# Kernel optimization log

Hardware: AMD Instinct MI355X
Metric: run time of the kernel (lower is better)

## Reference

```python
import jax, jax.numpy as jnp
import numpy as np

NU = 100_000   # users
NI = 100_000   # items
D  = 64        # embedding_size
NR = 1_000_000 # rate edges (user->item)
NL = 500_000   # link edges (user->user)
NEG_SLOPE = 0.2


def setup_inputs() -> dict:
    key = jax.random.key(0)
    ks = iter(jax.random.split(key, 40))
    s1 = 1.0 / np.sqrt(D)      # fan-in D
    s2 = 1.0 / np.sqrt(2 * D)  # fan-in 2D
    def nrm(shape, scale):
        return (jax.random.normal(next(ks), shape, jnp.float32) * scale).astype(jnp.float32)
    def idx(n, hi):
        return jax.random.randint(next(ks), (n,), 0, hi, jnp.int32)
    inp = {
        "user_emb": nrm((NU, D), 0.1),
        "item_emb": nrm((NI, D), 0.1),
        "rate_src": idx(NR, NU), "rate_dst": idx(NR, NI),
        "link_src": idx(NL, NU), "link_dst": idx(NL, NU),
        "neg_rate_src": idx(NR, NU), "neg_rate_dst": idx(NR, NI),
        "neg_link_src": idx(NL, NU), "neg_link_dst": idx(NL, NU),
        "lambda_max": jnp.full((), 2.0, jnp.float32),
        "gat_Wsrc": nrm((5, D, D), s1), "gat_bsrc": nrm((5, D), s1),
        "gat_Wdst": nrm((5, D, D), s1), "gat_bdst": nrm((5, D), s1),
        "gat_attn": nrm((5, D), s1),
        "W_out": nrm((2 * D, D), s2), "b_out": nrm((D,), s2),
        "cheb_W": nrm((3, D, D), s1), "cheb_b": nrm((D,), s1),
        "Wc": nrm((2 * D, D), s2), "bc": nrm((D,), s2),
        "Ws": nrm((2 * D, D), s2), "bs": nrm((D,), s2),
        "WpP": nrm((2 * D, D), s2), "bpP": nrm((D,), s2),
        "WpS": nrm((2 * D, D), s2), "bpS": nrm((D,), s2),
    }
    return inp


def _gatv2(Wsrc, bsrc, Wdst, bdst, attn, h_src, h_dst, src, dst, n_dst):
    """DGL GATv2Conv, num_heads=1, head dim squeezed. Returns [n_dst, D]."""
    fs = h_src @ Wsrc + bsrc            # [Ns, D]
    fd = h_dst @ Wdst + bdst            # [Nd, D]
    e = jax.nn.leaky_relu(fs[src] + fd[dst], NEG_SLOPE)  # [E, D]
    s = e @ attn                        # [E]
    m = jax.ops.segment_max(s, dst, num_segments=n_dst)
    ex = jnp.exp(s - m[dst])
    den = jax.ops.segment_sum(ex, dst, num_segments=n_dst)
    alpha = ex / den[dst]               # edge softmax per dst node
    return jax.ops.segment_sum(alpha[:, None] * fs[src], dst, num_segments=n_dst)


def _forward(user_emb, item_emb, rate_src, rate_dst, link_src, link_dst,
             neg_rate_src, neg_rate_dst, neg_link_src, neg_link_dst,
             lambda_max, gat_Wsrc, gat_bsrc, gat_Wdst, gat_bdst, gat_attn,
             W_out, b_out, cheb_W, cheb_b, Wc, bc, Ws, bs, WpP, bpP, WpS, bpS):
    def gat(i, h_src, h_dst, src, dst, n_dst):
        return _gatv2(gat_Wsrc[i], gat_bsrc[i], gat_Wdst[i], gat_bdst[i],
                      gat_attn[i], h_src, h_dst, src, dst, n_dst)

    # ---- SpatialAttentionLayer_GAT ----
    h1_item = gat(0, user_emb, item_emb, rate_src, rate_dst, NI)      # layer1[rate]
    h2_user = gat(1, item_emb, user_emb, rate_dst, rate_src, NU)      # layer1[rated-by]
    item_infl = gat(2, h1_item, user_emb, rate_dst, rate_src, NU)     # layer2[rated-by]
    social_item = gat(3, h2_user, user_emb, link_src, link_dst, NU)   # layer2[link]
    user_pref = jnp.concatenate([item_infl, social_item], axis=1) @ W_out + b_out

    # ---- SpectralAttentionLayer: ChebConv(k=3) on social graph + GATv2 ----
    indeg = jax.ops.segment_sum(jnp.ones((NL,), jnp.float32), link_dst, num_segments=NU)
    dinv = jnp.maximum(indeg, 1.0) ** -0.5
    def ahat(x):  # D^{-1/2} A D^{-1/2} x over link edges
        msg = (x * dinv[:, None])[link_src]
        return dinv[:, None] * jax.ops.segment_sum(msg, link_dst, num_segments=NU)
    re = 2.0 / lambda_max
    T0 = user_emb
    rst = T0 @ cheb_W[0]
    h = ahat(T0)
    T1 = -re * h + T0 * (re - 1.0)
    rst = rst + T1 @ cheb_W[1]
    h = ahat(T1)
    T2 = -2.0 * re * h + 2.0 * (re - 1.0) * T1 - T0
    rst = rst + T2 @ cheb_W[2] + cheb_b
    user_social = gat(4, rst, rst, link_src, link_dst, NU)

    # ---- MutualisicLayer ----
    h_uP = jnp.concatenate([user_pref, user_emb], axis=1) @ Wc + bc
    h_uS = jnp.concatenate([user_social, user_emb], axis=1) @ Ws + bs
    h_m = h_uP * h_uS
    h_mP = h_m * jax.nn.softmax(h_uP, axis=1)
    h_mS = h_m * jax.nn.softmax(h_uS, axis=1)
    h_miu_mP = jnp.concatenate([h_mP, h_uP], axis=1)
    h_miu_mS = jnp.concatenate([h_mS, h_uS], axis=1)

    # ---- PredictionLayer ----
    h_new_P = h_miu_mP @ WpP + bpP
    h_new_S = h_miu_mS @ WpS + bpS

    # ---- HeteroDotProductPredictor (u_dot_v per edge) ----
    pos_rate = jnp.sum(h_new_P[rate_src] * item_emb[rate_dst], axis=-1)
    neg_rate = jnp.sum(h_new_P[neg_rate_src] * item_emb[neg_rate_dst], axis=-1)
    pos_link = jnp.sum(h_new_S[link_src] * user_emb[link_dst], axis=-1)
    neg_link = jnp.sum(h_new_S[neg_link_src] * user_emb[neg_link_dst], axis=-1)
    return pos_rate, neg_rate, pos_link, neg_link


def reference(user_emb, item_emb, rate_src, rate_dst, link_src, link_dst,
              neg_rate_src, neg_rate_dst, neg_link_src, neg_link_dst,
              lambda_max, gat_Wsrc, gat_bsrc, gat_Wdst, gat_bdst, gat_attn,
              W_out, b_out, cheb_W, cheb_b, Wc, bc, Ws, bs, WpP, bpP, WpS, bpS):
    return _forward(user_emb, item_emb, rate_src, rate_dst, link_src, link_dst,
                    neg_rate_src, neg_rate_dst, neg_link_src, neg_link_dst,
                    lambda_max, gat_Wsrc, gat_bsrc, gat_Wdst, gat_bdst, gat_attn,
                    W_out, b_out, cheb_W, cheb_b, Wc, bc, Ws, bs, WpP, bpP, WpS, bpS)
```

## Files before the change

### kernel.cpp

```cpp
#include <hip/hip_runtime.h>


#define LRELU_SLOPE 0.2f
#define MFMA_BLOCKS 1024
#define EDGE_BLOCKS 2048

typedef unsigned short u16;
typedef unsigned int uint32;
typedef __attribute__((ext_vector_type(8))) short short8;
typedef __attribute__((ext_vector_type(4))) float f32x4;

__device__ __forceinline__ float b2f(u16 u) {
  return __uint_as_float(((uint32)u) << 16);
}
__device__ __forceinline__ u16 f2b(float f) {
  uint32 u = __float_as_uint(f);
  uint32 r = (u + 0x7fffu + ((u >> 16) & 1u)) >> 16;
  return (u16)r;
}
__device__ __forceinline__ float blo(uint32 p) { return __uint_as_float(p << 16); }
__device__ __forceinline__ float bhi(uint32 p) { return __uint_as_float(p & 0xffff0000u); }
__device__ __forceinline__ uint32 packb(float lo, float hi) {
  return (uint32)f2b(lo) | ((uint32)f2b(hi) << 16);
}

__global__ void cvt_k(const float4* __restrict__ X, ushort4* __restrict__ Y, int n4) {
  const int stride = gridDim.x * blockDim.x;
  for (int i = blockIdx.x * blockDim.x + threadIdx.x; i < n4; i += stride) {
    const float4 v = X[i];
    ushort4 o;
    o.x = f2b(v.x); o.y = f2b(v.y); o.z = f2b(v.z); o.w = f2b(v.w);
    Y[i] = o;
  }
}

__global__ void wfrag_k(const float* __restrict__ W, u16* __restrict__ fb, int nmat) {
  const int total = nmat * 4096;
  const int stride = gridDim.x * blockDim.x;
  for (int i = blockIdx.x * blockDim.x + threadIdx.x; i < total; i += stride) {
    const int mat = i >> 12, rem = i & 4095;
    const int l = rem >> 6, r = rem & 63;
    const int kc = r >> 5, cb = (r >> 3) & 3, j = r & 7;
    const int k = kc * 32 + ((l >> 4) & 3) * 8 + j;
    const int col = cb * 16 + (l & 15);
    fb[i] = f2b(W[(size_t)mat * 4096 + k * 64 + col]);
  }
}

template <int NIN>
__global__ void mfma_g_k(const u16* __restrict__ X0, const u16* __restrict__ X1,
                         const u16* __restrict__ X2,
                         const u16* __restrict__ F0, const u16* __restrict__ F1,
                         const u16* __restrict__ F2,
                         const float* __restrict__ b, u16* __restrict__ Y, int N) {
  const int lane = threadIdx.x & 63;
  const int gw = (blockIdx.x * blockDim.x + threadIdx.x) >> 6;
  const int nw = (gridDim.x * blockDim.x) >> 6;
  const int lo = lane & 15, hi = lane >> 4;
  short8 bf[NIN][2][4];
#pragma unroll
  for (int i = 0; i < NIN; ++i) {
    const u16* Fi = (i == 0) ? F0 : ((i == 1) ? F1 : F2);
#pragma unroll
    for (int kc = 0; kc < 2; ++kc)
#pragma unroll
      for (int cb = 0; cb < 4; ++cb)
        bf[i][kc][cb] = *(const short8*)(Fi + (size_t)lane * 64 + kc * 32 + cb * 8);
  }
  float bcol[4];
#pragma unroll
  for (int cb = 0; cb < 4; ++cb) bcol[cb] = b[cb * 16 + lo];
  const int ntile = (N + 15) >> 4;
  for (int t = gw; t < ntile; t += nw) {
    int arow = t * 16 + lo;
    if (arow >= N) arow = N - 1;
    f32x4 acc[4];
#pragma unroll
    for (int cb = 0; cb < 4; ++cb) {
      acc[cb][0] = bcol[cb]; acc[cb][1] = bcol[cb];
      acc[cb][2] = bcol[cb]; acc[cb][3] = bcol[cb];
    }
#pragma unroll
    for (int i = 0; i < NIN; ++i) {
      const u16* Xi = (i == 0) ? X0 : ((i == 1) ? X1 : X2);
      const short8 a0 = *(const short8*)(Xi + (size_t)arow * 64 + hi * 8);
      const short8 a1 = *(const short8*)(Xi + (size_t)arow * 64 + 32 + hi * 8);
#pragma unroll
      for (int cb = 0; cb < 4; ++cb)
        acc[cb] = __builtin_amdgcn_mfma_f32_16x16x32_bf16(a0, bf[i][0][cb], acc[cb], 0, 0, 0);
#pragma unroll
      for (int cb = 0; cb < 4; ++cb)
        acc[cb] = __builtin_amdgcn_mfma_f32_16x16x32_bf16(a1, bf[i][1][cb], acc[cb], 0, 0, 0);
    }
#pragma unroll
    for (int cb = 0; cb < 4; ++cb) {
#pragma unroll
      for (int j = 0; j < 4; ++j) {
        const int row = t * 16 + hi * 4 + j;
        if (row < N) Y[(size_t)row * 64 + cb * 16 + lo] = f2b(acc[cb][j]);
      }
    }
  }
}

__global__ void mfma_g2_k(const u16* __restrict__ X,
                          const u16* __restrict__ F0, const u16* __restrict__ F1,
                          const float* __restrict__ b0, const float* __restrict__ b1,
                          u16* __restrict__ Y0, u16* __restrict__ Y1, int N) {
  const int lane = threadIdx.x & 63;
  const int gw = (blockIdx.x * blockDim.x + threadIdx.x) >> 6;
  const int nw = (gridDim.x * blockDim.x) >> 6;
  const int lo = lane & 15, hi = lane >> 4;
  short8 bfA[2][4], bfB[2][4];
#pragma unroll
  for (int kc = 0; kc < 2; ++kc)
#pragma unroll
    for (int cb = 0; cb < 4; ++cb) {
      bfA[kc][cb] = *(const short8*)(F0 + (size_t)lane * 64 + kc * 32 + cb * 8);
      bfB[kc][cb] = *(const short8*)(F1 + (size_t)lane * 64 + kc * 32 + cb * 8);
    }
  float bc0[4], bc1[4];
#pragma unroll
  for (int cb = 0; cb < 4; ++cb) { bc0[cb] = b0[cb * 16 + lo]; bc1[cb] = b1[cb * 16 + lo]; }
  const int ntile = (N + 15) >> 4;
  for (int t = gw; t < ntile; t += nw) {
    int arow = t * 16 + lo;
    if (arow >= N) arow = N - 1;
    const short8 a0 = *(const short8*)(X + (size_t)arow * 64 + hi * 8);
    const short8 a1 = *(const short8*)(X + (size_t)arow * 64 + 32 + hi * 8);
    f32x4 accA[4], accB[4];
#pragma unroll
    for (int cb = 0; cb < 4; ++cb) {
      accA[cb][0] = bc0[cb]; accA[cb][1] = bc0[cb]; accA[cb][2] = bc0[cb]; accA[cb][3] = bc0[cb];
      accB[cb][0] = bc1[cb]; accB[cb][1] = bc1[cb]; accB[cb][2] = bc1[cb]; accB[cb][3] = bc1[cb];
    }
#pragma unroll
    for (int cb = 0; cb < 4; ++cb) {
      accA[cb] = __builtin_amdgcn_mfma_f32_16x16x32_bf16(a0, bfA[0][cb], accA[cb], 0, 0, 0);
      accA[cb] = __builtin_amdgcn_mfma_f32_16x16x32_bf16(a1, bfA[1][cb], accA[cb], 0, 0, 0);
      accB[cb] = __builtin_amdgcn_mfma_f32_16x16x32_bf16(a0, bfB[0][cb], accB[cb], 0, 0, 0);
      accB[cb] = __builtin_amdgcn_mfma_f32_16x16x32_bf16(a1, bfB[1][cb], accB[cb], 0, 0, 0);
    }
#pragma unroll
    for (int cb = 0; cb < 4; ++cb) {
#pragma unroll
      for (int j = 0; j < 4; ++j) {
        const int row = t * 16 + hi * 4 + j;
        if (row < N) {
          Y0[(size_t)row * 64 + cb * 16 + lo] = f2b(accA[cb][j]);
          Y1[(size_t)row * 64 + cb * 16 + lo] = f2b(accB[cb][j]);
        }
      }
    }
  }
}

__global__ void hist_k(const int* __restrict__ key, int* __restrict__ cnt, int E) {
  const int e = blockIdx.x * blockDim.x + threadIdx.x;
  if (e < E) atomicAdd(cnt + key[e], 1);
}

__global__ void scan1_k(const int* __restrict__ in, int* __restrict__ out,
                        int* __restrict__ bsum, int n) {
  __shared__ int tmp[256];
  const int t = threadIdx.x;
  const int base = blockIdx.x * 1024 + t * 4;
  int v0 = (base + 0 < n) ? in[base + 0] : 0;
  int v1 = (base + 1 < n) ? in[base + 1] : 0;
  int v2 = (base + 2 < n) ? in[base + 2] : 0;
  int v3 = (base + 3 < n) ? in[base + 3] : 0;
  const int s = v0 + v1 + v2 + v3;
  tmp[t] = s;
  __syncthreads();
  for (int off = 1; off < 256; off <<= 1) {
    const int x = (t >= off) ? tmp[t - off] : 0;
    __syncthreads();
    tmp[t] += x;
    __syncthreads();
  }
  const int excl = tmp[t] - s;
  if (t == 255) bsum[blockIdx.x] = tmp[255];
  if (base + 0 < n) out[base + 0] = excl;
  if (base + 1 < n) out[base + 1] = excl + v0;
  if (base + 2 < n) out[base + 2] = excl + v0 + v1;
  if (base + 3 < n) out[base + 3] = excl + v0 + v1 + v2;
}
__global__ void scan2_k(int* __restrict__ bsum, int nb) {
  if (threadIdx.x == 0) {
    int acc = 0;
    for (int i = 0; i < nb; ++i) { const int v = bsum[i]; bsum[i] = acc; acc += v; }
  }
}
__global__ void scan3_k(int* __restrict__ out, const int* __restrict__ bsum, int n) {
  const int i = blockIdx.x * blockDim.x + threadIdx.x;
  if (i < n) out[i] += bsum[i >> 10];
}

__global__ void scatter_k(const int* __restrict__ key, const int* __restrict__ other,
                          int* __restrict__ cursor, int* __restrict__ srt, int E) {
  const int e = blockIdx.x * blockDim.x + threadIdx.x;
  if (e < E) {
    const int p = atomicAdd(cursor + key[e], 1);
    srt[p] = other[e];
  }
}

__global__ void gat32_k(const u16* __restrict__ fs, const u16* __restrict__ fd,
                        const float* __restrict__ attn,
                        const int* __restrict__ rowptr, const int* __restrict__ nbr,
                        u16* __restrict__ out, int N) {
  const int lane = threadIdx.x & 63;
  const int l = lane & 31, half = lane >> 5;
  const int wid = (blockIdx.x * blockDim.x + threadIdx.x) >> 6;
  const int nw = (gridDim.x * blockDim.x) >> 6;
  const float awlo = attn[2 * l], awhi = attn[2 * l + 1];
  const uint32* fs32 = (const uint32*)fs;
  const uint32* fd32 = (const uint32*)fd;
  uint32* out32 = (uint32*)out;
  for (int n0 = wid * 2; n0 < N; n0 += nw * 2) {
    const int n = n0 + half;
    const bool act = n < N;
    const int beg = act ? rowptr[n] : 0;
    const int end = act ? rowptr[n + 1] : 0;
    float fdlo = 0.0f, fdhi = 0.0f;
    if (act) {
      const uint32 fp = fd32[(size_t)n * 32 + l];
      fdlo = blo(fp); fdhi = bhi(fp);
    }
    float aclo = 0.0f, achi = 0.0f, den = 0.0f;
    int e = beg;
    for (; e + 1 < end; e += 2) {
      const int s0 = nbr[e], s1 = nbr[e + 1];
      const uint32 f0 = fs32[(size_t)s0 * 32 + l];
      const uint32 f1 = fs32[(size_t)s1 * 32 + l];
      const float f0l = blo(f0), f0h = bhi(f0);
      const float f1l = blo(f1), f1h = bhi(f1);
      float v0l = f0l + fdlo; v0l = v0l > 0.0f ? v0l : LRELU_SLOPE * v0l;
      float v0h = f0h + fdhi; v0h = v0h > 0.0f ? v0h : LRELU_SLOPE * v0h;
      float v1l = f1l + fdlo; v1l = v1l > 0.0f ? v1l : LRELU_SLOPE * v1l;
      float v1h = f1h + fdhi; v1h = v1h > 0.0f ? v1h : LRELU_SLOPE * v1h;
      float p0 = fmaf(v0l, awlo, v0h * awhi);
      float p1 = fmaf(v1l, awlo, v1h * awhi);
#pragma unroll
      for (int o = 16; o; o >>= 1) {
        p0 += __shfl_xor(p0, o, 64);
        p1 += __shfl_xor(p1, o, 64);
      }
      const float e0 = __expf(p0), e1 = __expf(p1);
      den += e0 + e1;
      aclo = fmaf(e0, f0l, aclo); achi = fmaf(e0, f0h, achi);
      aclo = fmaf(e1, f1l, aclo); achi = fmaf(e1, f1h, achi);
    }
    if (e < end) {
      const int s0 = nbr[e];
      const uint32 f0 = fs32[(size_t)s0 * 32 + l];
      const float f0l = blo(f0), f0h = bhi(f0);
      float v0l = f0l + fdlo; v0l = v0l > 0.0f ? v0l : LRELU_SLOPE * v0l;
      float v0h = f0h + fdhi; v0h = v0h > 0.0f ? v0h : LRELU_SLOPE * v0h;
      float p0 = fmaf(v0l, awlo, v0h * awhi);
#pragma unroll
      for (int o = 16; o; o >>= 1) p0 += __shfl_xor(p0, o, 64);
      const float e0 = __expf(p0);
      den += e0;
      aclo = fmaf(e0, f0l, aclo); achi = fmaf(e0, f0h, achi);
    }
    const float inv = den > 0.0f ? 1.0f / den : 0.0f;
    if (act) out32[(size_t)n * 32 + l] = packb(aclo * inv, achi * inv);
  }
}

template <int MODE>
__global__ void cheb32_k(const u16* __restrict__ x, const u16* __restrict__ T0,
                         const u16* __restrict__ Tp, const float* __restrict__ dinv,
                         const float* __restrict__ lam,
                         const int* __restrict__ rowptr, const int* __restrict__ nbr,
                         u16* __restrict__ outT, int N) {
  const float re = 2.0f / lam[0];
  const int lane = threadIdx.x & 63;
  const int l = lane & 31, half = lane >> 5;
  const int wid = (blockIdx.x * blockDim.x + threadIdx.x) >> 6;
  const int nw = (gridDim.x * blockDim.x) >> 6;
  const uint32* x32 = (const uint32*)x;
  const uint32* T032 = (const uint32*)T0;
  const uint32* Tp32 = (const uint32*)Tp;
  uint32* o32 = (uint32*)outT;
  for (int n0 = wid * 2; n0 < N; n0 += nw * 2) {
    const int n = n0 + half;
    const bool act = n < N;
    const int beg = act ? rowptr[n] : 0;
    const int end = act ? rowptr[n + 1] : 0;
    float aclo = 0.0f, achi = 0.0f;
    int e = beg;
    for (; e + 1 < end; e += 2) {
      const int s0 = nbr[e], s1 = nbr[e + 1];
      const uint32 f0 = x32[(size_t)s0 * 32 + l];
      const uint32 f1 = x32[(size_t)s1 * 32 + l];
      const float d0 = dinv[s0], d1 = dinv[s1];
      aclo = fmaf(blo(f0), d0, aclo); achi = fmaf(bhi(f0), d0, achi);
      aclo = fmaf(blo(f1), d1, aclo); achi = fmaf(bhi(f1), d1, achi);
    }
    if (e < end) {
      const int s0 = nbr[e];
      const uint32 f0 = x32[(size_t)s0 * 32 + l];
      const float d0 = dinv[s0];
      aclo = fmaf(blo(f0), d0, aclo); achi = fmaf(bhi(f0), d0, achi);
    }
    if (!act) continue;
    const float dn = dinv[n];
    const float hl = aclo * dn, hh = achi * dn;
    float rl, rh;
    if (MODE == 1) {
      const uint32 t0 = T032[(size_t)n * 32 + l];
      rl = -re * hl + (re - 1.0f) * blo(t0);
      rh = -re * hh + (re - 1.0f) * bhi(t0);
    } else {
      const uint32 t0 = T032[(size_t)n * 32 + l];
      const uint32 tp = Tp32[(size_t)n * 32 + l];
      rl = -2.0f * re * hl + 2.0f * (re - 1.0f) * blo(tp) - blo(t0);
      rh = -2.0f * re * hh + 2.0f * (re - 1.0f) * bhi(tp) - bhi(t0);
    }
    o32[(size_t)n * 32 + l] = packb(rl, rh);
  }
}

__global__ void dinv_k(const int* __restrict__ rowptr, float* __restrict__ dinv, int N) {
  const int i = blockIdx.x * blockDim.x + threadIdx.x;
  if (i < N) {
    const float deg = (float)(rowptr[i + 1] - rowptr[i]);
    dinv[i] = rsqrtf(fmaxf(deg, 1.0f));
  }
}

__global__ void mut_k(const u16* __restrict__ hP, const u16* __restrict__ hS,
                      u16* __restrict__ mP, u16* __restrict__ mS, int N) {
  const int lane = threadIdx.x & 63;
  const int u = (blockIdx.x * blockDim.x + threadIdx.x) >> 6;
  if (u >= N) return;
  const float p = b2f(hP[(size_t)u * 64 + lane]);
  const float s = b2f(hS[(size_t)u * 64 + lane]);
  const float m = p * s;
  float mxp = p, mxs = s;
#pragma unroll
  for (int o = 32; o; o >>= 1) {
    mxp = fmaxf(mxp, __shfl_xor(mxp, o, 64));
    mxs = fmaxf(mxs, __shfl_xor(mxs, o, 64));
  }
  const float ep = __expf(p - mxp);
  const float es = __expf(s - mxs);
  float sp = ep, ss = es;
#pragma unroll
  for (int o = 32; o; o >>= 1) {
    sp += __shfl_xor(sp, o, 64);
    ss += __shfl_xor(ss, o, 64);
  }
  mP[(size_t)u * 64 + lane] = f2b(m * (ep / sp));
  mS[(size_t)u * 64 + lane] = f2b(m * (es / ss));
}

__global__ void dot32_k(const u16* __restrict__ A, const u16* __restrict__ Bm,
                        const int* __restrict__ src, const int* __restrict__ dst,
                        float* __restrict__ out, int E) {
  const int lane = threadIdx.x & 63;
  const int l = lane & 31, half = lane >> 5;
  const int wid = (blockIdx.x * blockDim.x + threadIdx.x) >> 6;
  const int nw = (gridDim.x * blockDim.x) >> 6;
  const uint32* A32 = (const uint32*)A;
  const uint32* B32 = (const uint32*)Bm;
  for (int e0 = wid * 4; e0 < E; e0 += nw * 4) {
    const int eA = e0 + half;
    const int eB = e0 + 2 + half;
    const int eAc = eA < E ? eA : E - 1;
    const int eBc = eB < E ? eB : E - 1;
    const int sA = src[eAc], dA = dst[eAc];
    const int sB = src[eBc], dB = dst[eBc];
    const uint32 a0 = A32[(size_t)sA * 32 + l];
    const uint32 b0 = B32[(size_t)dA * 32 + l];
    const uint32 a1 = A32[(size_t)sB * 32 + l];
    const uint32 b1 = B32[(size_t)dB * 32 + l];
    float p0 = fmaf(blo(a0), blo(b0), bhi(a0) * bhi(b0));
    float p1 = fmaf(blo(a1), blo(b1), bhi(a1) * bhi(b1));
#pragma unroll
    for (int o = 16; o; o >>= 1) {
      p0 += __shfl_xor(p0, o, 64);
      p1 += __shfl_xor(p1, o, 64);
    }
    if (l == 0) {
      if (eA < E) out[eA] = p0;
      if (eB < E) out[eB] = p1;
    }
  }
}


static void build_csr(const int* key, const int* other, int E, int N,
                      int* rowptr, int* srt, int* cursor, int* bsum,
                      hipStream_t stream) {
  const int n1 = N + 1;
  hipMemsetAsync(cursor, 0, (size_t)n1 * 4, stream);
  hist_k<<<(E + 255) / 256, 256, 0, stream>>>(key, cursor, E);
  const int nb = (n1 + 1023) / 1024;
  scan1_k<<<nb, 256, 0, stream>>>(cursor, rowptr, bsum, n1);
  scan2_k<<<1, 64, 0, stream>>>(bsum, nb);
  scan3_k<<<(n1 + 255) / 256, 256, 0, stream>>>(rowptr, bsum, n1);
  hipMemcpyAsync(cursor, rowptr, (size_t)N * 4, hipMemcpyDeviceToDevice, stream);
  scatter_k<<<(E + 255) / 256, 256, 0, stream>>>(key, other, cursor, srt, E);
}

extern "C" void kernel_launch(void* const* d_in, const int* in_sizes, int n_in,
                              void* d_out, int out_size, void* d_ws, size_t ws_size,
                              hipStream_t stream) {
  const float* user_emb = (const float*)d_in[0];
  const float* item_emb = (const float*)d_in[1];
  const int* rate_src = (const int*)d_in[2];
  const int* rate_dst = (const int*)d_in[3];
  const int* link_src = (const int*)d_in[4];
  const int* link_dst = (const int*)d_in[5];
  const int* neg_rate_src = (const int*)d_in[6];
  const int* neg_rate_dst = (const int*)d_in[7];
  const int* neg_link_src = (const int*)d_in[8];
  const int* neg_link_dst = (const int*)d_in[9];
  const float* lam = (const float*)d_in[10];
  const float* gat_Wsrc = (const float*)d_in[11];
  const float* gat_bsrc = (const float*)d_in[12];
  const float* gat_Wdst = (const float*)d_in[13];
  const float* gat_bdst = (const float*)d_in[14];
  const float* gat_attn = (const float*)d_in[15];
  const float* W_out = (const float*)d_in[16];
  const float* b_out = (const float*)d_in[17];
  const float* cheb_W = (const float*)d_in[18];
  const float* cheb_b = (const float*)d_in[19];
  const float* Wc = (const float*)d_in[20];
  const float* bc = (const float*)d_in[21];
  const float* Wsm = (const float*)d_in[22];
  const float* bs = (const float*)d_in[23];
  const float* WpP = (const float*)d_in[24];
  const float* bpP = (const float*)d_in[25];
  const float* WpS = (const float*)d_in[26];
  const float* bpS = (const float*)d_in[27];

  const int NU = in_sizes[0] / 64;
  const int NI = in_sizes[1] / 64;
  const int NR = in_sizes[2];
  const int NL = in_sizes[4];
  const int NMAX = NU > NI ? NU : NI;
  const size_t MAT = (size_t)NMAX * 64;
  const int FR = 4096;

  u16* ub = (u16*)d_ws;
  u16* ib = ub + (size_t)NU * 64;
  u16* B0 = ib + (size_t)NI * 64;
  u16* B1 = B0 + MAT;
  u16* B2 = B1 + MAT;
  u16* B3 = B2 + MAT;
  u16* B4 = B3 + MAT;
  u16* B5 = B4 + MAT;
  u16* B6 = B5 + MAT;
  u16* B7 = B6 + MAT;
  u16* fb = B7 + MAT;
  u16* fbWsrc = fb;
  u16* fbWdst = fb + 5 * FR;
  u16* fbWout = fb + 10 * FR;
  u16* fbCheb = fb + 12 * FR;
  u16* fbWc = fb + 15 * FR;
  u16* fbWsm = fb + 17 * FR;
  u16* fbWpP = fb + 19 * FR;
  u16* fbWpS = fb + 21 * FR;
  int* ip = (int*)(fb + 23 * FR);
  int* rp_rd = ip;
  int* rp_rs = rp_rd + (NI + 1);
  int* rp_ld = rp_rs + (NU + 1);
  int* srt_rd = rp_ld + (NU + 1);
  int* srt_rs = srt_rd + NR;
  int* srt_ld = srt_rs + NR;
  int* cursor = srt_ld + NL;
  int* bsum = cursor + (NMAX + 1);
  float* dinv = (float*)(bsum + 256);

  const int B64 = 64;

  cvt_k<<<1024, 256, 0, stream>>>((const float4*)user_emb, (ushort4*)ub, NU * 16);
  cvt_k<<<1024, 256, 0, stream>>>((const float4*)item_emb, (ushort4*)ib, NI * 16);
  wfrag_k<<<20, 256, 0, stream>>>(gat_Wsrc, fbWsrc, 5);
  wfrag_k<<<20, 256, 0, stream>>>(gat_Wdst, fbWdst, 5);
  wfrag_k<<<8, 256, 0, stream>>>(W_out, fbWout, 2);
  wfrag_k<<<12, 256, 0, stream>>>(cheb_W, fbCheb, 3);
  wfrag_k<<<8, 256, 0, stream>>>(Wc, fbWc, 2);
  wfrag_k<<<8, 256, 0, stream>>>(Wsm, fbWsm, 2);
  wfrag_k<<<8, 256, 0, stream>>>(WpP, fbWpP, 2);
  wfrag_k<<<8, 256, 0, stream>>>(WpS, fbWpS, 2);

  build_csr(rate_dst, rate_src, NR, NI, rp_rd, srt_rd, cursor, bsum, stream);
  build_csr(rate_src, rate_dst, NR, NU, rp_rs, srt_rs, cursor, bsum, stream);
  build_csr(link_dst, link_src, NL, NU, rp_ld, srt_ld, cursor, bsum, stream);

  mfma_g2_k<<<MFMA_BLOCKS, 256, 0, stream>>>(ub, fbWsrc + 0 * FR, fbWdst + 1 * FR,
      gat_bsrc + 0 * B64, gat_bdst + 1 * B64, B0, B1, NU);
  mfma_g2_k<<<MFMA_BLOCKS, 256, 0, stream>>>(ub, fbWdst + 2 * FR, fbWdst + 3 * FR,
      gat_bdst + 2 * B64, gat_bdst + 3 * B64, B2, B3, NU);
  mfma_g2_k<<<MFMA_BLOCKS, 256, 0, stream>>>(ib, fbWdst + 0 * FR, fbWsrc + 1 * FR,
      gat_bdst + 0 * B64, gat_bsrc + 1 * B64, B4, B5, NI);

  gat32_k<<<EDGE_BLOCKS, 256, 0, stream>>>(B0, B4, gat_attn + 0 * B64, rp_rd, srt_rd, B6, NI);
  gat32_k<<<EDGE_BLOCKS, 256, 0, stream>>>(B5, B1, gat_attn + 1 * B64, rp_rs, srt_rs, B7, NU);

  mfma_g_k<1><<<MFMA_BLOCKS, 256, 0, stream>>>(B6, nullptr, nullptr,
      fbWsrc + 2 * FR, nullptr, nullptr, gat_bsrc + 2 * B64, B0, NI);
  gat32_k<<<EDGE_BLOCKS, 256, 0, stream>>>(B0, B2, gat_attn + 2 * B64, rp_rs, srt_rs, B4, NU);

  mfma_g_k<1><<<MFMA_BLOCKS, 256, 0, stream>>>(B7, nullptr, nullptr,
      fbWsrc + 3 * FR, nullptr, nullptr, gat_bsrc + 3 * B64, B5, NU);
  gat32_k<<<EDGE_BLOCKS, 256, 0, stream>>>(B5, B3, gat_attn + 3 * B64, rp_ld, srt_ld, B2, NU);

  mfma_g_k<2><<<MFMA_BLOCKS, 256, 0, stream>>>(B4, B2, nullptr,
      fbWout + 0 * FR, fbWout + 1 * FR, nullptr, b_out, B0, NU);

  dinv_k<<<(NU + 255) / 256, 256, 0, stream>>>(rp_ld, dinv, NU);
  cheb32_k<1><<<EDGE_BLOCKS, 256, 0, stream>>>(ub, ub, nullptr, dinv, lam,
                                               rp_ld, srt_ld, B5, NU);
  cheb32_k<2><<<EDGE_BLOCKS, 256, 0, stream>>>(B5, ub, B5, dinv, lam,
                                               rp_ld, srt_ld, B3, NU);
  mfma_g_k<3><<<MFMA_BLOCKS, 256, 0, stream>>>(ub, B5, B3,
      fbCheb + 0 * FR, fbCheb + 1 * FR, fbCheb + 2 * FR, cheb_b, B6, NU);

  mfma_g2_k<<<MFMA_BLOCKS, 256, 0, stream>>>(B6, fbWsrc + 4 * FR, fbWdst + 4 * FR,
      gat_bsrc + 4 * B64, gat_bdst + 4 * B64, B4, B2, NU);
  gat32_k<<<EDGE_BLOCKS, 256, 0, stream>>>(B4, B2, gat_attn + 4 * B64, rp_ld, srt_ld, B5, NU);

  mfma_g_k<2><<<MFMA_BLOCKS, 256, 0, stream>>>(B0, ub, nullptr,
      fbWc + 0 * FR, fbWc + 1 * FR, nullptr, bc, B4, NU);
  mfma_g_k<2><<<MFMA_BLOCKS, 256, 0, stream>>>(B5, ub, nullptr,
      fbWsm + 0 * FR, fbWsm + 1 * FR, nullptr, bs, B2, NU);
  mut_k<<<(NU + 3) / 4, 256, 0, stream>>>(B4, B2, B3, B7, NU);
  mfma_g_k<2><<<MFMA_BLOCKS, 256, 0, stream>>>(B3, B4, nullptr,
      fbWpP + 0 * FR, fbWpP + 1 * FR, nullptr, bpP, B0, NU);
  mfma_g_k<2><<<MFMA_BLOCKS, 256, 0, stream>>>(B7, B2, nullptr,
      fbWpS + 0 * FR, fbWpS + 1 * FR, nullptr, bpS, B5, NU);

  float* out = (float*)d_out;
  dot32_k<<<EDGE_BLOCKS, 256, 0, stream>>>(B0, ib, rate_src, rate_dst, out, NR);
  dot32_k<<<EDGE_BLOCKS, 256, 0, stream>>>(B0, ib, neg_rate_src, neg_rate_dst, out + NR, NR);
  dot32_k<<<EDGE_BLOCKS, 256, 0, stream>>>(B5, ub, link_src, link_dst, out + 2 * (size_t)NR, NL);
  dot32_k<<<EDGE_BLOCKS, 256, 0, stream>>>(B5, ub, neg_link_src, neg_link_dst, out + 2 * (size_t)NR + NL, NL);
}
```

Before: 1.017 ms.

## Batch independent launches and share CSR traversal across two GAT layers

Merges the two embedding conversions into one kernel and the eight weight-fragment kernels into one. Pairs independent MFMA GEMMs and edge dot-product kernels into single launches by splitting the grid in half. Fuses two GAT aggregations that walk the same rate_src CSR into one kernel, so the neighbour indices are read once and two feature rows are gathered per edge. The aim is to cut launch overhead and tail idle time; the fused GAT kernel needs more registers per lane and runs two serial softmax chains together, and it assumes the weight fragment buffer fb is laid out contiguously.

Result: faster. 992.7 us (-2.4%).

```diff
diff --git a/kernel.cpp b/kernel.cpp
--- a/kernel.cpp
+++ b/kernel.cpp
@@ -24,26 +24,95 @@
   return (uint32)f2b(lo) | ((uint32)f2b(hi) << 16);
 }
 
-__global__ void cvt_k(const float4* __restrict__ X, ushort4* __restrict__ Y, int n4) {
+__global__ void cvt2_k(const float4* __restrict__ A, ushort4* __restrict__ Ya, int n4a,
+                       const float4* __restrict__ B, ushort4* __restrict__ Yb, int n4b) {
   const int stride = gridDim.x * blockDim.x;
-  for (int i = blockIdx.x * blockDim.x + threadIdx.x; i < n4; i += stride) {
-    const float4 v = X[i];
+  const int total = n4a + n4b;
+  for (int i = blockIdx.x * blockDim.x + threadIdx.x; i < total; i += stride) {
+    const bool first = i < n4a;
+    const float4 v = first ? A[i] : B[i - n4a];
     ushort4 o;
     o.x = f2b(v.x); o.y = f2b(v.y); o.z = f2b(v.z); o.w = f2b(v.w);
-    Y[i] = o;
-  }
-}
-
-__global__ void wfrag_k(const float* __restrict__ W, u16* __restrict__ fb, int nmat) {
-  const int total = nmat * 4096;
+    if (first) Ya[i] = o; else Yb[i - n4a] = o;
+  }
+}
+
+__global__ void wfrag_all_k(const float* __restrict__ Wsrc, const float* __restrict__ Wdst,
+                            const float* __restrict__ Wout, const float* __restrict__ Wch,
+                            const float* __restrict__ Wc, const float* __restrict__ Wsm,
+                            const float* __restrict__ WpP, const float* __restrict__ WpS,
+                            u16* __restrict__ fb) {
+  const int total = 23 * 4096;
   const int stride = gridDim.x * blockDim.x;
   for (int i = blockIdx.x * blockDim.x + threadIdx.x; i < total; i += stride) {
     const int mat = i >> 12, rem = i & 4095;
+    const float* W;
+    int m;
+    if (mat < 5)       { W = Wsrc; m = mat; }
+    else if (mat < 10) { W = Wdst; m = mat - 5; }
+    else if (mat < 12) { W = Wout; m = mat - 10; }
+    else if (mat < 15) { W = Wch;  m = mat - 12; }
+    else if (mat < 17) { W = Wc;   m = mat - 15; }
+    else if (mat < 19) { W = Wsm;  m = mat - 17; }
+    else if (mat < 21) { W = WpP;  m = mat - 19; }
+    else               { W = WpS;  m = mat - 21; }
     const int l = rem >> 6, r = rem & 63;
     const int kc = r >> 5, cb = (r >> 3) & 3, j = r & 7;
     const int k = kc * 32 + ((l >> 4) & 3) * 8 + j;
     const int col = cb * 16 + (l & 15);
-    fb[i] = f2b(W[(size_t)mat * 4096 + k * 64 + col]);
+    fb[i] = f2b(W[(size_t)m * 4096 + k * 64 + col]);
+  }
+}
+
+template <int NIN>
+__device__ __forceinline__ void mfma_body(const u16* X0, const u16* X1, const u16* X2,
+                                          const u16* F0, const u16* F1, const u16* F2,
+                                          const float* b, u16* Y, int N,
+                                          int gw, int nw, int lane) {
+  const int lo = lane & 15, hi = lane >> 4;
+  short8 bf[NIN][2][4];
+#pragma unroll
+  for (int i = 0; i < NIN; ++i) {
+    const u16* Fi = (i == 0) ? F0 : ((i == 1) ? F1 : F2);
+#pragma unroll
+    for (int kc = 0; kc < 2; ++kc)
+#pragma unroll
+      for (int cb = 0; cb < 4; ++cb)
+        bf[i][kc][cb] = *(const short8*)(Fi + (size_t)lane * 64 + kc * 32 + cb * 8);
+  }
+  float bcol[4];
+#pragma unroll
+  for (int cb = 0; cb < 4; ++cb) bcol[cb] = b[cb * 16 + lo];
+  const int ntile = (N + 15) >> 4;
+  for (int t = gw; t < ntile; t += nw) {
+    int arow = t * 16 + lo;
+    if (arow >= N) arow = N - 1;
+    f32x4 acc[4];
+#pragma unroll
+    for (int cb = 0; cb < 4; ++cb) {
+      acc[cb][0] = bcol[cb]; acc[cb][1] = bcol[cb];
+      acc[cb][2] = bcol[cb]; acc[cb][3] = bcol[cb];
+    }
+#pragma unroll
+    for (int i = 0; i < NIN; ++i) {
+      const u16* Xi = (i == 0) ? X0 : ((i == 1) ? X1 : X2);
+      const short8 a0 = *(const short8*)(Xi + (size_t)arow * 64 + hi * 8);
+      const short8 a1 = *(const short8*)(Xi + (size_t)arow * 64 + 32 + hi * 8);
+#pragma unroll
+      for (int cb = 0; cb < 4; ++cb)
+        acc[cb] = __builtin_amdgcn_mfma_f32_16x16x32_bf16(a0, bf[i][0][cb], acc[cb], 0, 0, 0);
+#pragma unroll
+      for (int cb = 0; cb < 4; ++cb)
+        acc[cb] = __builtin_amdgcn_mfma_f32_16x16x32_bf16(a1, bf[i][1][cb], acc[cb], 0, 0, 0);
+    }
+#pragma unroll
+    for (int cb = 0; cb < 4; ++cb) {
+#pragma unroll
+      for (int j = 0; j < 4; ++j) {
+        const int row = t * 16 + hi * 4 + j;
+        if (row < N) Y[(size_t)row * 64 + cb * 16 + lo] = f2b(acc[cb][j]);
+      }
+    }
   }
 }
 
@@ -56,51 +125,7 @@
   const int lane = threadIdx.x & 63;
   const int gw = (blockIdx.x * blockDim.x + threadIdx.x) >> 6;
   const int nw = (gridDim.x * blockDim.x) >> 6;
-  const int lo = lane & 15, hi = lane >> 4;
-  short8 bf[NIN][2][4];
-#pragma unroll
-  for (int i = 0; i < NIN; ++i) {
-    const u16* Fi = (i == 0) ? F0 : ((i == 1) ? F1 : F2);
-#pragma unroll
-    for (int kc = 0; kc < 2; ++kc)
-#pragma unroll
-      for (int cb = 0; cb < 4; ++cb)
-        bf[i][kc][cb] = *(const short8*)(Fi + (size_t)lane * 64 + kc * 32 + cb * 8);
-  }
-  float bcol[4];
-#pragma unroll
-  for (int cb = 0; cb < 4; ++cb) bcol[cb] = b[cb * 16 + lo];
-  const int ntile = (N + 15) >> 4;
-  for (int t = gw; t < ntile; t += nw) {
-    int arow = t * 16 + lo;
-    if (arow >= N) arow = N - 1;
-    f32x4 acc[4];
-#pragma unroll
-    for (int cb = 0; cb < 4; ++cb) {
-      acc[cb][0] = bcol[cb]; acc[cb][1] = bcol[cb];
-      acc[cb][2] = bcol[cb]; acc[cb][3] = bcol[cb];
-    }
-#pragma unroll
-    for (int i = 0; i < NIN; ++i) {
-      const u16* Xi = (i == 0) ? X0 : ((i == 1) ? X1 : X2);
-      const short8 a0 = *(const short8*)(Xi + (size_t)arow * 64 + hi * 8);
-      const short8 a1 = *(const short8*)(Xi + (size_t)arow * 64 + 32 + hi * 8);
-#pragma unroll
-      for (int cb = 0; cb < 4; ++cb)
-        acc[cb] = __builtin_amdgcn_mfma_f32_16x16x32_bf16(a0, bf[i][0][cb], acc[cb], 0, 0, 0);
-#pragma unroll
-      for (int cb = 0; cb < 4; ++cb)
-        acc[cb] = __builtin_amdgcn_mfma_f32_16x16x32_bf16(a1, bf[i][1][cb], acc[cb], 0, 0, 0);
-    }
-#pragma unroll
-    for (int cb = 0; cb < 4; ++cb) {
-#pragma unroll
-      for (int j = 0; j < 4; ++j) {
-        const int row = t * 16 + hi * 4 + j;
-        if (row < N) Y[(size_t)row * 64 + cb * 16 + lo] = f2b(acc[cb][j]);
-      }
-    }
-  }
+  mfma_body<NIN>(X0, X1, X2, F0, F1, F2, b, Y, N, gw, nw, lane);
 }
 
 __global__ void mfma_g2_k(const u16* __restrict__ X,
@@ -153,6 +178,22 @@
       }
     }
   }
+}
+
+__global__ void mfma_pair_k(const u16* __restrict__ Xa0, const u16* __restrict__ Xa1,
+                            const u16* __restrict__ Fa0, const u16* __restrict__ Fa1,
+                            const float* __restrict__ ba, u16* __restrict__ Ya, int Na,
+                            const u16* __restrict__ Xb0, const u16* __restrict__ Xb1,
+                            const u16* __restrict__ Fb0, const u16* __restrict__ Fb1,
+                            const float* __restrict__ bb, u16* __restrict__ Yb, int Nb) {
+  const int lane = threadIdx.x & 63;
+  const int halfg = gridDim.x >> 1;
+  const bool jobA = (int)blockIdx.x < halfg;
+  const int bid = jobA ? blockIdx.x : blockIdx.x - halfg;
+  const int gw = (bid * blockDim.x + threadIdx.x) >> 6;
+  const int nw = (halfg * blockDim.x) >> 6;
+  if (jobA) mfma_body<2>(Xa0, Xa1, nullptr, Fa0, Fa1, nullptr, ba, Ya, Na, gw, nw, lane);
+  else      mfma_body<2>(Xb0, Xb1, nullptr, Fb0, Fb1, nullptr, bb, Yb, Nb, gw, nw, lane);
 }
 
 __global__ void hist_k(const int* __restrict__ key, int* __restrict__ cnt, int E) {
@@ -266,6 +307,68 @@
     }
     const float inv = den > 0.0f ? 1.0f / den : 0.0f;
     if (act) out32[(size_t)n * 32 + l] = packb(aclo * inv, achi * inv);
+  }
+}
+
+__global__ void gat12_k(const u16* __restrict__ fsA, const u16* __restrict__ fdA,
+                        const float* __restrict__ attnA, u16* __restrict__ outA,
+                        const u16* __restrict__ fsB, const u16* __restrict__ fdB,
+                        const float* __restrict__ attnB, u16* __restrict__ outB,
+                        const int* __restrict__ rowptr, const int* __restrict__ nbr, int N) {
+  const int lane = threadIdx.x & 63;
+  const int l = lane & 31, half = lane >> 5;
+  const int wid = (blockIdx.x * blockDim.x + threadIdx.x) >> 6;
+  const int nw = (gridDim.x * blockDim.x) >> 6;
+  const float awAlo = attnA[2 * l], awAhi = attnA[2 * l + 1];
+  const float awBlo = attnB[2 * l], awBhi = attnB[2 * l + 1];
+  const uint32* fsA32 = (const uint32*)fsA;
+  const uint32* fdA32 = (const uint32*)fdA;
+  const uint32* fsB32 = (const uint32*)fsB;
+  const uint32* fdB32 = (const uint32*)fdB;
+  uint32* outA32 = (uint32*)outA;
+  uint32* outB32 = (uint32*)outB;
+  for (int n0 = wid * 2; n0 < N; n0 += nw * 2) {
+    const int n = n0 + half;
+    const bool act = n < N;
+    const int beg = act ? rowptr[n] : 0;
+    const int end = act ? rowptr[n + 1] : 0;
+    float fdAlo = 0.f, fdAhi = 0.f, fdBlo = 0.f, fdBhi = 0.f;
+    if (act) {
+      const uint32 fa = fdA32[(size_t)n * 32 + l];
+      const uint32 fbv = fdB32[(size_t)n * 32 + l];
+      fdAlo = blo(fa); fdAhi = bhi(fa);
+      fdBlo = blo(fbv); fdBhi = bhi(fbv);
+    }
+    float acAlo = 0.f, acAhi = 0.f, denA = 0.f;
+    float acBlo = 0.f, acBhi = 0.f, denB = 0.f;
+    for (int e = beg; e < end; ++e) {
+      const int s0 = nbr[e];
+      const uint32 fa = fsA32[(size_t)s0 * 32 + l];
+      const uint32 fbv = fsB32[(size_t)s0 * 32 + l];
+      const float fal = blo(fa), fah = bhi(fa);
+      const float fbl = blo(fbv), fbh = bhi(fbv);
+      float vAl = fal + fdAlo; vAl = vAl > 0.f ? vAl : LRELU_SLOPE * vAl;
+      float vAh = fah + fdAhi; vAh = vAh > 0.f ? vAh : LRELU_SLOPE * vAh;
+      float vBl = fbl + fdBlo; vBl = vBl > 0.f ? vBl : LRELU_SLOPE * vBl;
+      float vBh = fbh + fdBhi; vBh = vBh > 0.f ? vBh : LRELU_SLOPE * vBh;
+      float pA = fmaf(vAl, awAlo, vAh * awAhi);
+      float pB = fmaf(vBl, awBlo, vBh * awBhi);
+#pragma unroll
+      for (int o = 16; o; o >>= 1) {
+        pA += __shfl_xor(pA, o, 64);
+        pB += __shfl_xor(pB, o, 64);
+      }
+      const float eA = __expf(pA), eB = __expf(pB);
+      denA += eA; denB += eB;
+      acAlo = fmaf(eA, fal, acAlo); acAhi = fmaf(eA, fah, acAhi);
+      acBlo = fmaf(eB, fbl, acBlo); acBhi = fmaf(eB, fbh, acBhi);
+    }
+    if (act) {
+      const float iA = denA > 0.f ? 1.0f / denA : 0.f;
+      const float iB = denB > 0.f ? 1.0f / denB : 0.f;
+      outA32[(size_t)n * 32 + l] = packb(acAlo * iA, acAhi * iA);
+      outB32[(size_t)n * 32 + l] = packb(acBlo * iB, acBhi * iB);
+    }
   }
 }
 
@@ -357,15 +460,10 @@
   mS[(size_t)u * 64 + lane] = f2b(m * (es / ss));
 }
 
-__global__ void dot32_k(const u16* __restrict__ A, const u16* __restrict__ Bm,
-                        const int* __restrict__ src, const int* __restrict__ dst,
-                        float* __restrict__ out, int E) {
-  const int lane = threadIdx.x & 63;
-  const int l = lane & 31, half = lane >> 5;
-  const int wid = (blockIdx.x * blockDim.x + threadIdx.x) >> 6;
-  const int nw = (gridDim.x * blockDim.x) >> 6;
-  const uint32* A32 = (const uint32*)A;
-  const uint32* B32 = (const uint32*)Bm;
+__device__ __forceinline__ void dot_body(const uint32* A32, const uint32* B32,
+                                         const int* src, const int* dst,
+                                         float* out, int E,
+                                         int wid, int nw, int l, int half) {
   for (int e0 = wid * 4; e0 < E; e0 += nw * 4) {
     const int eA = e0 + half;
     const int eB = e0 + 2 + half;
@@ -389,6 +487,24 @@
       if (eB < E) out[eB] = p1;
     }
   }
+}
+
+__global__ void dot_pair_k(const u16* __restrict__ A, const u16* __restrict__ Bm,
+                           const int* __restrict__ src1, const int* __restrict__ dst1,
+                           float* __restrict__ out1, int E1,
+                           const int* __restrict__ src2, const int* __restrict__ dst2,
+                           float* __restrict__ out2, int E2) {
+  const int lane = threadIdx.x & 63;
+  const int l = lane & 31, half = lane >> 5;
+  const int halfg = gridDim.x >> 1;
+  const bool job1 = (int)blockIdx.x < halfg;
+  const int bid = job1 ? blockIdx.x : blockIdx.x - halfg;
+  const int wid = (bid * blockDim.x + threadIdx.x) >> 6;
+  const int nw = (halfg * blockDim.x) >> 6;
+  const uint32* A32 = (const uint32*)A;
+  const uint32* B32 = (const uint32*)Bm;
+  if (job1) dot_body(A32, B32, src1, dst1, out1, E1, wid, nw, l, half);
+  else      dot_body(A32, B32, src2, dst2, out2, E2, wid, nw, l, half);
 }
 
 
@@ -478,16 +594,10 @@
 
   const int B64 = 64;
 
-  cvt_k<<<1024, 256, 0, stream>>>((const float4*)user_emb, (ushort4*)ub, NU * 16);
-  cvt_k<<<1024, 256, 0, stream>>>((const float4*)item_emb, (ushort4*)ib, NI * 16);
-  wfrag_k<<<20, 256, 0, stream>>>(gat_Wsrc, fbWsrc, 5);
-  wfrag_k<<<20, 256, 0, stream>>>(gat_Wdst, fbWdst, 5);
-  wfrag_k<<<8, 256, 0, stream>>>(W_out, fbWout, 2);
-  wfrag_k<<<12, 256, 0, stream>>>(cheb_W, fbCheb, 3);
-  wfrag_k<<<8, 256, 0, stream>>>(Wc, fbWc, 2);
-  wfrag_k<<<8, 256, 0, stream>>>(Wsm, fbWsm, 2);
-  wfrag_k<<<8, 256, 0, stream>>>(WpP, fbWpP, 2);
-  wfrag_k<<<8, 256, 0, stream>>>(WpS, fbWpS, 2);
+  cvt2_k<<<2048, 256, 0, stream>>>((const float4*)user_emb, (ushort4*)ub, NU * 16,
+                                   (const float4*)item_emb, (ushort4*)ib, NI * 16);
+  wfrag_all_k<<<368, 256, 0, stream>>>(gat_Wsrc, gat_Wdst, W_out, cheb_W,
+                                       Wc, Wsm, WpP, WpS, fb);
 
   build_csr(rate_dst, rate_src, NR, NI, rp_rd, srt_rd, cursor, bsum, stream);
   build_csr(rate_src, rate_dst, NR, NU, rp_rs, srt_rs, cursor, bsum, stream);
@@ -501,11 +611,13 @@
       gat_bdst + 0 * B64, gat_bsrc + 1 * B64, B4, B5, NI);
 
   gat32_k<<<EDGE_BLOCKS, 256, 0, stream>>>(B0, B4, gat_attn + 0 * B64, rp_rd, srt_rd, B6, NI);
-  gat32_k<<<EDGE_BLOCKS, 256, 0, stream>>>(B5, B1, gat_attn + 1 * B64, rp_rs, srt_rs, B7, NU);
 
   mfma_g_k<1><<<MFMA_BLOCKS, 256, 0, stream>>>(B6, nullptr, nullptr,
       fbWsrc + 2 * FR, nullptr, nullptr, gat_bsrc + 2 * B64, B0, NI);
-  gat32_k<<<EDGE_BLOCKS, 256, 0, stream>>>(B0, B2, gat_attn + 2 * B64, rp_rs, srt_rs, B4, NU);
+
+  gat12_k<<<EDGE_BLOCKS, 256, 0, stream>>>(B5, B1, gat_attn + 1 * B64, B7,
+                                           B0, B2, gat_attn + 2 * B64, B4,
+                                           rp_rs, srt_rs, NU);
 
   mfma_g_k<1><<<MFMA_BLOCKS, 256, 0, stream>>>(B7, nullptr, nullptr,
       fbWsrc + 3 * FR, nullptr, nullptr, gat_bsrc + 3 * B64, B5, NU);
@@ -526,19 +638,19 @@
       gat_bsrc + 4 * B64, gat_bdst + 4 * B64, B4, B2, NU);
   gat32_k<<<EDGE_BLOCKS, 256, 0, stream>>>(B4, B2, gat_attn + 4 * B64, rp_ld, srt_ld, B5, NU);
 
-  mfma_g_k<2><<<MFMA_BLOCKS, 256, 0, stream>>>(B0, ub, nullptr,
-      fbWc + 0 * FR, fbWc + 1 * FR, nullptr, bc, B4, NU);
-  mfma_g_k<2><<<MFMA_BLOCKS, 256, 0, stream>>>(B5, ub, nullptr,
-      fbWsm + 0 * FR, fbWsm + 1 * FR, nullptr, bs, B2, NU);
+  mfma_pair_k<<<2 * MFMA_BLOCKS, 256, 0, stream>>>(
+      B0, ub, fbWc + 0 * FR, fbWc + 1 * FR, bc, B4, NU,
+      B5, ub, fbWsm + 0 * FR, fbWsm + 1 * FR, bs, B2, NU);
   mut_k<<<(NU + 3) / 4, 256, 0, stream>>>(B4, B2, B3, B7, NU);
-  mfma_g_k<2><<<MFMA_BLOCKS, 256, 0, stream>>>(B3, B4, nullptr,
-      fbWpP + 0 * FR, fbWpP + 1 * FR, nullptr, bpP, B0, NU);
-  mfma_g_k<2><<<MFMA_BLOCKS, 256, 0, stream>>>(B7, B2, nullptr,
-      fbWpS + 0 * FR, fbWpS + 1 * FR, nullptr, bpS, B5, NU);
+  mfma_pair_k<<<2 * MFMA_BLOCKS, 256, 0, stream>>>(
+      B3, B4, fbWpP + 0 * FR, fbWpP + 1 * FR, bpP, B0, NU,
+      B7, B2, fbWpS + 0 * FR, fbWpS + 1 * FR, bpS, B5, NU);
 
   float* out = (float*)d_out;
-  dot32_k<<<EDGE_BLOCKS, 256, 0, stream>>>(B0, ib, rate_src, rate_dst, out, NR);
-  dot32_k<<<EDGE_BLOCKS, 256, 0, stream>>>(B0, ib, neg_rate_src, neg_rate_dst, out + NR, NR);
-  dot32_k<<<EDGE_BLOCKS, 256, 0, stream>>>(B5, ub, link_src, link_dst, out + 2 * (size_t)NR, NL);
-  dot32_k<<<EDGE_BLOCKS, 256, 0, stream>>>(B5, ub, neg_link_src, neg_link_dst, out + 2 * (size_t)NR + NL, NL);
-}
+  dot_pair_k<<<EDGE_BLOCKS, 256, 0, stream>>>(B0, ib, rate_src, rate_dst, out, NR,
+                                              neg_rate_src, neg_rate_dst, out + NR, NR);
+  dot_pair_k<<<EDGE_BLOCKS, 256, 0, stream>>>(B5, ub, link_src, link_dst,
+                                              out + 2 * (size_t)NR, NL,
+                                              neg_link_src, neg_link_dst,
+                                              out + 2 * (size_t)NR + NL, NL);
+}
```
